# Kernel optimization log

Measured on AMD Instinct MI355X. Metric: run time of the kernel, lower is better.

## Reference

```python
import jax, jax.numpy as jnp
import numpy as np

J = 24          # SMPL_NR_JOINTS
H = 24          # hidden_dim
D_IN = 3        # input_dim (xyz)
SMPL_PARENTS = [-1, 0, 0, 0, 1, 2, 3, 4, 5, 6, 7, 8, 9, 9, 9, 12, 13, 14, 16, 17, 18, 19, 20, 21]

def _build_A():
    # undirected kinematic tree + self loops, row-normalized (mean aggregation)
    M = np.zeros((J, J), np.float32)
    for child, parent in enumerate(SMPL_PARENTS):
        if parent >= 0:
            M[child, parent] = 1.0
            M[parent, child] = 1.0
    M += np.eye(J, dtype=np.float32)
    M /= M.sum(axis=1, keepdims=True)
    return jnp.asarray(M)

A_NORM = _build_A()  # [J, J]

def setup_inputs() -> dict:
    key = jax.random.key(0)
    ks = jax.random.split(key, 12)
    B, S, T = 2048, 24, 24
    g = lambda k, shape, s=0.1: jax.random.normal(k, shape, dtype=jnp.float32) * s
    return {
        "src": g(ks[0], (B, S, J, D_IN), 1.0),
        "tgt": g(ks[1], (B, T, J, D_IN), 1.0),
        "We": g(ks[2], (H, D_IN)), "be": jnp.zeros((H,), jnp.float32),
        # gate order: 0=i, 1=f, 2=c, 3=o
        "Wxl": g(ks[3], (4, H, H)), "bxl": jnp.zeros((4, H), jnp.float32),
        "Wxr": g(ks[4], (4, H, H)),
        "Whl": g(ks[5], (4, H, H)), "bhl": jnp.zeros((4, H), jnp.float32),
        "Whr": g(ks[6], (4, H, H)),
        "wg": g(ks[7], (3, H)),   # peephole weights for i, f, o
        "bg": jnp.zeros((4, H), jnp.float32),
        "Wd": g(ks[8], (D_IN * J, H * J)), "bd": jnp.zeros((D_IN * J,), jnp.float32),
    }

def _gconv(x, Wl, bl, Wr):
    # x: [B, J, D]; mean-aggregate over fixed 24-node graph, then l(agg) + r(x)
    agg = jnp.einsum('ij,bjd->bid', A_NORM, x)
    return agg @ Wl.T + bl + x @ Wr.T

def _cell(X, h, c, Wxl, bxl, Wxr, Whl, bhl, Whr, wg, bg):
    gx = lambda g: _gconv(X, Wxl[g], bxl[g], Wxr[g])
    gh = lambda g: _gconv(h, Whl[g], bhl[g], Whr[g])
    i = jax.nn.sigmoid(gx(0) + gh(0) + wg[0] * c + bg[0])
    f = jax.nn.sigmoid(gx(1) + gh(1) + wg[1] * c + bg[1])
    c_new = f * c + i * jnp.tanh(gx(2) + gh(2) + bg[2])
    o = jax.nn.sigmoid(gx(3) + gh(3) + wg[2] * c_new + bg[3])
    h_new = o * jnp.tanh(c_new)
    return o, h_new, c_new

def reference(src, tgt, We, be, Wxl, bxl, Wxr, Whl, bhl, Whr, wg, bg, Wd, bd):
    B, S = src.shape[0], src.shape[1]
    T = tgt.shape[1]
    params = (Wxl, bxl, Wxr, Whl, bhl, Whr, wg, bg)
    enc = lambda x: jax.nn.relu(x @ We.T + be)  # [B, J, H]

    # --- warm-up over last 24 src frames (deterministic: encode only first step) ---
    X0 = enc(src[:, S - 24])
    h = jnp.zeros((B, J, H), src.dtype)
    c = jnp.zeros((B, J, H), src.dtype)
    out, h, c = _cell(X0, h, c, *params)

    def warm_step(carry, _):
        o_, h_, c_ = carry
        o_, h_, c_ = _cell(o_, h_, c_, *params)
        return (o_, h_, c_), None
    (out, h, c), _ = jax.lax.scan(warm_step, (out, h, c), None, length=23)

    # --- decode T steps: first input is enc(tgt[:,0]), then feed previous out ---
    out0, h, c = _cell(enc(tgt[:, 0]), h, c, *params)

    def dec_step(carry, _):
        o_, h_, c_ = carry
        o2, h2, c2 = _cell(o_, h_, c_, *params)
        return (o2, h2, c2), o2
    _, rest = jax.lax.scan(dec_step, (out0, h, c), None, length=T - 1)  # [T-1, B, J, H]

    seq = jnp.concatenate([out0[None], rest], axis=0)            # [T, B, J, H]
    outs = seq.transpose(1, 0, 2, 3).reshape(B, T, J * H)        # [B, T, 576]
    return outs @ Wd.T + bd                                      # [B, T, 72]
```

## Files before the change

kernel.cpp:

```cpp
#include <hip/hip_runtime.h>


typedef short  s16x8 __attribute__((ext_vector_type(8)));
typedef float  f32x4 __attribute__((ext_vector_type(4)));
typedef _Float16 f16x8 __attribute__((ext_vector_type(8)));

#define TPB 192
#define NB 2
#define PQ_OFF 0
#define UO_OFF 19968
#define SMEM_SZ 26880

#define BAR() do { asm volatile("s_waitcnt lgkmcnt(0)" ::: "memory"); \
                   __builtin_amdgcn_s_barrier(); } while (0)

__device__ __forceinline__ unsigned short f2h(float f) {
    _Float16 h = (_Float16)f;
    return *(unsigned short*)&h;
}
__device__ __forceinline__ unsigned int pkrtz(float a, float b) {
    auto h = __builtin_amdgcn_cvt_pkrtz(a, b);
    return *(unsigned int*)&h;
}
__device__ __forceinline__ float frcp(float x) { return __builtin_amdgcn_rcpf(x); }
__device__ __forceinline__ float sigm(float x) {
    float t = __expf(-x);
    return frcp(1.0f + t);
}
__device__ __forceinline__ float tanh_(float x) {
    float xc = fmaxf(x, -30.f);
    float t = __expf(-2.f * xc);
    return (1.f - t) * frcp(1.f + t);
}

extern "C" __global__ void __launch_bounds__(TPB, 3)
gclstm_main(const float* __restrict__ src,
            const float* __restrict__ tgt,
            const float* __restrict__ We,
            const float* __restrict__ be,
            const float* __restrict__ Wxl,
            const float* __restrict__ bxl,
            const float* __restrict__ Wxr,
            const float* __restrict__ Whl,
            const float* __restrict__ bhl,
            const float* __restrict__ Whr,
            const float* __restrict__ wg,
            const float* __restrict__ bg,
            unsigned short* __restrict__ seqh)
{
    __shared__ __align__(16) char smem[SMEM_SZ];
    unsigned short* PQt  = (unsigned short*)(smem + PQ_OFF);
    unsigned short* UO   = (unsigned short*)(smem + UO_OFF);
    unsigned int*   UO32 = (unsigned int*)(smem + UO_OFF);

    const int tid = threadIdx.x;
    const int b0 = blockIdx.x * NB;
    const int lane = tid & 63, wid = tid >> 6;
    const int l15 = lane & 15, quad = lane >> 4;

    const int par[24] = {-1,0,0,0,1,2,3,4,5,6,7,8,9,9,9,12,13,14,16,17,18,19,20,21};

    f16x8 w1f[4][2];
#pragma unroll
    for (int cj = 0; cj < 4; ++cj) {
        int np = (wid * 4 + cj) * 16 + l15;
        int path = np >= 96 ? 1 : 0;
        int nn = np - path * 96;
        int g = nn / 24, d = nn - g * 24;
        const float* Wx = path ? Wxr : Wxl;
        const float* Wh = path ? Whr : Whl;
#pragma unroll
        for (int kt = 0; kt < 2; ++kt) {
            f16x8 f;
#pragma unroll
            for (int kk = 0; kk < 8; ++kk) {
                int k = kt * 32 + quad * 8 + kk;
                float v = 0.f;
                if (k < 48) {
                    int df = k >> 1;
                    v = (k & 1) ? Wh[g * 576 + d * 24 + df] : Wx[g * 576 + d * 24 + df];
                }
                f[kk] = (_Float16)v;
            }
            w1f[cj][kt] = f;
        }
    }

    f16x8 mf[3];
    {
        int i = wid * 16 + l15;
        int si = i / 24, ji = i - si * 24;
        int cnt = 1 + (par[ji] >= 0 ? 1 : 0);
#pragma unroll
        for (int ch = 0; ch < 24; ++ch) cnt += (par[ch] == ji) ? 1 : 0;
        float cntf = (float)cnt;
#pragma unroll
        for (int kt = 0; kt < 3; ++kt) {
            f16x8 f;
#pragma unroll
            for (int kk = 0; kk < 8; ++kk) {
                int jp = kt * 32 + quad * 8 + kk;
                int sj = jp / 48;
                int rem = jp - sj * 48;
                int pz = rem / 24;
                int j = rem - pz * 24;
                float v = 0.f;
                if (sj == si) {
                    if (pz == 0) v = (j == ji || par[j] == ji || par[ji] == j) ? 1.f : 0.f;
                    else         v = (j == ji) ? cntf : 0.f;
                }
                f[kk] = (_Float16)v;
            }
            mf[kt] = f;
        }
    }

    const int d1 = l15;
    const int d2 = 16 + (l15 & 7);
    const bool lo = l15 < 8;
    float bC1[4], bC2[4], wv1[3], wv2[3];
#pragma unroll
    for (int g = 0; g < 4; ++g) {
        bC1[g] = bxl[g * 24 + d1] + bhl[g * 24 + d1] + bg[g * 24 + d1];
        bC2[g] = bxl[g * 24 + d2] + bhl[g * 24 + d2] + bg[g * 24 + d2];
    }
#pragma unroll
    for (int p = 0; p < 3; ++p) { wv1[p] = wg[p * 24 + d1]; wv2[p] = wg[p * 24 + d2]; }

    int rowR[4];
    float iwR[4];
    unsigned int sb[4];
#pragma unroll
    for (int rr = 0; rr < 4; ++rr) {
        int row = wid * 16 + quad * 4 + rr;
        rowR[rr] = row;
        int j = row % 24;
        int cnt = 1 + (par[j] >= 0 ? 1 : 0);
#pragma unroll
        for (int ch = 0; ch < 24; ++ch) cnt += (par[ch] == j) ? 1 : 0;
        iwR[rr] = cnt == 2 ? 0.5f : cnt == 3 ? (1.f / 3.f) : cnt == 4 ? 0.25f : 0.2f;
        sb[rr] = (unsigned int)((b0 + row / 24) * 13824 + j * 24);
    }
    int row2v[2]; float iw2v[2]; unsigned int sb2v[2];
#pragma unroll
    for (int e = 0; e < 2; ++e) {
        int rsel = lo ? e : e + 2;
        row2v[e] = rowR[rsel]; iw2v[e] = iwR[rsel]; sb2v[e] = sb[rsel];
    }

    float c1[4] = {0.f, 0.f, 0.f, 0.f};
    float c2[2] = {0.f, 0.f};

#pragma unroll
    for (int t = 0; t < 3; ++t) {
        int task = tid + t * TPB;
        int row = task / 12, dp = task - row * 12;
        int b = b0 + row / 24, j = row % 24;
        const float* sp = src + (size_t)b * 1728 + j * 3;
        float s0 = sp[0], s1 = sp[1], s2 = sp[2];
        int d = 2 * dp;
        float x0 = be[d] + s0 * We[d * 3] + s1 * We[d * 3 + 1] + s2 * We[d * 3 + 2];
        float x1 = be[d + 1] + s0 * We[d * 3 + 3] + s1 * We[d * 3 + 4] + s2 * We[d * 3 + 5];
        x0 = fmaxf(x0, 0.f); x1 = fmaxf(x1, 0.f);
        uint2 wv; wv.x = pkrtz(x0, 0.f); wv.y = pkrtz(x1, 0.f);
        *(uint2*)(UO32 + row * 36 + 2 * dp) = wv;
    }
    {
        int row = tid >> 2, c = tid & 3;
        uint2 z; z.x = 0u; z.y = 0u;
        *(uint2*)(UO32 + row * 36 + 24 + 2 * c) = z;
    }
    __syncthreads();

    for (int s = 0; s < 48; ++s) {
        if (s == 24) {
#pragma unroll
            for (int t = 0; t < 3; ++t) {
                int task = tid + t * TPB;
                int row = task / 12, dp = task - row * 12;
                int b = b0 + row / 24, j = row % 24;
                const float* tp = tgt + (size_t)b * 1728 + j * 3;
                float s0 = tp[0], s1 = tp[1], s2 = tp[2];
                int d = 2 * dp;
                float x0 = be[d] + s0 * We[d * 3] + s1 * We[d * 3 + 1] + s2 * We[d * 3 + 2];
                float x1 = be[d + 1] + s0 * We[d * 3 + 3] + s1 * We[d * 3 + 4]
                         + s2 * We[d * 3 + 5];
                x0 = fmaxf(x0, 0.f); x1 = fmaxf(x1, 0.f);
                UO[row * 72 + 4 * dp] = f2h(x0);
                UO[row * 72 + 4 * dp + 2] = f2h(x1);
            }
            BAR();
        }

        f32x4 acc1[3][4];
#pragma unroll
        for (int rt = 0; rt < 3; ++rt)
#pragma unroll
            for (int cj = 0; cj < 4; ++cj) acc1[rt][cj] = (f32x4)0.f;
#pragma unroll
        for (int kt = 0; kt < 2; ++kt) {
            f16x8 a[3];
#pragma unroll
            for (int rt = 0; rt < 3; ++rt)
                a[rt] = *(const f16x8*)(UO + (rt * 16 + l15) * 72 + kt * 32 + quad * 8);
#pragma unroll
            for (int rt = 0; rt < 3; ++rt)
#pragma unroll
                for (int cj = 0; cj < 4; ++cj)
                    acc1[rt][cj] = __builtin_amdgcn_mfma_f32_16x16x32_f16(a[rt], w1f[cj][kt], acc1[rt][cj], 0, 0, 0);
        }
#pragma unroll
        for (int rt = 0; rt < 3; ++rt)
#pragma unroll
            for (int cj = 0; cj < 4; ++cj) {
                int np = (wid * 4 + cj) * 16 + l15;
                int path = np >= 96;
                int nn = np - (path ? 96 : 0);
                int jg = rt * 16 + quad * 4;
                int col = (path ? 24 : 0) + jg + (jg >= 24 ? 24 : 0);
                uint2 wv;
                wv.x = pkrtz(acc1[rt][cj][0], acc1[rt][cj][1]);
                wv.y = pkrtz(acc1[rt][cj][2], acc1[rt][cj][3]);
                *(uint2*)(PQt + nn * 104 + col) = wv;
            }
        BAR();

        f32x4 acc2[6];
#pragma unroll
        for (int nt = 0; nt < 6; ++nt) acc2[nt] = (f32x4)0.f;
#pragma unroll
        for (int kt = 0; kt < 3; ++kt) {
            if (kt == 2 && wid == 0) continue;
            if (kt == 0 && wid == 2) continue;
            f16x8 bf[6];
#pragma unroll
            for (int nt = 0; nt < 6; ++nt)
                bf[nt] = *(const f16x8*)(PQt + (nt * 16 + l15) * 104 + kt * 32 + quad * 8);
#pragma unroll
            for (int nt = 0; nt < 6; ++nt)
                acc2[nt] = __builtin_amdgcn_mfma_f32_16x16x32_f16(mf[kt], bf[nt], acc2[nt], 0, 0, 0);
        }

        const int so = (s - 24) * 576;

#pragma unroll
        for (int rr = 0; rr < 4; ++rr) {
            float pf_s = __shfl_xor(lo ? acc2[2][rr] : acc2[1][rr], 8);
            float po_s = __shfl_xor(lo ? acc2[5][rr] : acc2[4][rr], 8);
            float iw = iwR[rr];
            int row = rowR[rr];
            float c = c1[rr];
            float pi = fmaf(iw, acc2[0][rr], bC1[0]);
            float pf = fmaf(iw, pf_s, bC1[1]);
            float pc = fmaf(iw, acc2[3][rr], bC1[2]);
            float po = fmaf(iw, po_s, bC1[3]);
            float iv = sigm(fmaf(wv1[0], c, pi));
            float fv = sigm(fmaf(wv1[1], c, pf));
            float cn = fmaf(fv, c, iv * tanh_(pc));
            float ov = sigm(fmaf(wv1[2], cn, po));
            c1[rr] = cn;
            float hv = ov * tanh_(cn);
            unsigned int pk = pkrtz(ov, hv);
            UO32[row * 36 + d1] = pk;
            if (s >= 24) seqh[sb[rr] + (unsigned int)(so + d1)] = (unsigned short)pk;
        }
#pragma unroll
        for (int e = 0; e < 2; ++e) {
            float sA = __shfl_xor(lo ? acc2[1][e + 2] : acc2[2][e], 8);
            float sB = __shfl_xor(lo ? acc2[4][e + 2] : acc2[5][e], 8);
            float g0 = lo ? acc2[1][e] : sA;
            float g1 = lo ? sA : acc2[2][e + 2];
            float g2 = lo ? acc2[4][e] : sB;
            float g3 = lo ? sB : acc2[5][e + 2];
            float iw = iw2v[e];
            int row = row2v[e];
            float c = c2[e];
            float pi = fmaf(iw, g0, bC2[0]);
            float pf = fmaf(iw, g1, bC2[1]);
            float pc = fmaf(iw, g2, bC2[2]);
            float po = fmaf(iw, g3, bC2[3]);
            float iv = sigm(fmaf(wv2[0], c, pi));
            float fv = sigm(fmaf(wv2[1], c, pf));
            float cn = fmaf(fv, c, iv * tanh_(pc));
            float ov = sigm(fmaf(wv2[2], cn, po));
            c2[e] = cn;
            float hv = ov * tanh_(cn);
            unsigned int pk = pkrtz(ov, hv);
            UO32[row * 36 + d2] = pk;
            if (s >= 24) seqh[sb2v[e] + (unsigned int)(so + d2)] = (unsigned short)pk;
        }
        BAR();
    }
}

extern "C" __global__ void __launch_bounds__(256)
wd_conv(const float* __restrict__ Wd, unsigned short* __restrict__ WdH)
{
    int i = blockIdx.x * 256 + threadIdx.x;
    if (i < 46080) {
        int n = i / 576, k = i - n * 576;
        WdH[i] = (n < 72) ? f2h(Wd[n * 576 + k]) : (unsigned short)0;
    }
}

__global__ void __launch_bounds__(256, 4)
gclstm_proj_reg(const unsigned short* __restrict__ seqh,
                const unsigned short* __restrict__ WdH,
                const float* __restrict__ bd,
                float* __restrict__ out)
{
    const int tid = threadIdx.x;
    const int R0 = blockIdx.x * 64;
    const int lane = tid & 63, wid = tid >> 6;
    const int l15 = lane & 15, quad = lane >> 4;

    const unsigned short* arow = seqh + (size_t)(R0 + wid * 16 + l15) * 576;
    f32x4 acc[5];
#pragma unroll
    for (int j = 0; j < 5; ++j) acc[j] = (f32x4)0.f;

#pragma unroll
    for (int kc = 0; kc < 576; kc += 96) {
        f16x8 a[3], b[5][3];
#pragma unroll
        for (int kt = 0; kt < 3; ++kt) {
            int koff = kc + kt * 32 + quad * 8;
            a[kt] = *(const f16x8*)(arow + koff);
#pragma unroll
            for (int j = 0; j < 5; ++j)
                b[j][kt] = *(const f16x8*)(WdH + (size_t)(j * 16 + l15) * 576 + koff);
        }
#pragma unroll
        for (int kt = 0; kt < 3; ++kt)
#pragma unroll
            for (int j = 0; j < 5; ++j)
                acc[j] = __builtin_amdgcn_mfma_f32_16x16x32_f16(a[kt], b[j][kt], acc[j], 0, 0, 0);
    }

#pragma unroll
    for (int j = 0; j < 5; ++j) {
        int n = j * 16 + l15;
        if (n < 72) {
            float bv = bd[n];
            int rbase = R0 + wid * 16 + quad * 4;
#pragma unroll
            for (int r = 0; r < 4; ++r)
                out[(size_t)(rbase + r) * 72 + (size_t)n] = acc[j][r] + bv;
        }
    }
}

__global__ void __launch_bounds__(256, 6)
gclstm_proj_lds(const unsigned short* __restrict__ seqh,
                const float* __restrict__ Wd,
                const float* __restrict__ bd,
                float* __restrict__ out)
{
    __shared__ unsigned short SQ[32 * 104];
    __shared__ unsigned short WH[80 * 104];

    const int tid = threadIdx.x;
    const int R0 = blockIdx.x * 32;
    const int lane = tid & 63, wid = tid >> 6;
    const int l15 = lane & 15, quad = lane >> 4;
    const int rt = wid & 1;
    const int c0 = (wid < 2) ? 0 : 3;
    const int nct = (wid < 2) ? 3 : 2;

    f32x4 acc[3];
#pragma unroll
    for (int j = 0; j < 3; ++j) acc[j] = (f32x4)0.f;

    for (int kc = 0; kc < 576; kc += 96) {
        __syncthreads();
        for (int i = tid; i < 384; i += 256) {
            int r = i / 12, c8 = i - r * 12;
            *(s16x8*)(&SQ[r * 104 + c8 * 8]) =
                *(const s16x8*)(seqh + (size_t)(R0 + r) * 576 + (size_t)(kc + c8 * 8));
        }
        for (int i = tid; i < 7680; i += 256) {
            int n = i / 96, kk = i - n * 96;
            float v = (n < 72) ? Wd[(size_t)n * 576 + (size_t)(kc + kk)] : 0.f;
            WH[n * 104 + kk] = f2h(v);
        }
        __syncthreads();
#pragma unroll
        for (int kt = 0; kt < 3; ++kt) {
            int koff = kt * 32 + quad * 8;
            f16x8 a = *(const f16x8*)(&SQ[(rt * 16 + l15) * 104 + koff]);
#pragma unroll
            for (int j = 0; j < 3; ++j) {
                if (j < nct) {
                    f16x8 b = *(const f16x8*)(&WH[((c0 + j) * 16 + l15) * 104 + koff]);
                    acc[j] = __builtin_amdgcn_mfma_f32_16x16x32_f16(a, b, acc[j], 0, 0, 0);
                }
            }
        }
    }

#pragma unroll
    for (int j = 0; j < 3; ++j) {
        if (j < nct) {
            int n = (c0 + j) * 16 + l15;
            if (n < 72) {
                float bv = bd[n];
                int rbase = R0 + rt * 16 + quad * 4;
#pragma unroll
                for (int r = 0; r < 4; ++r)
                    out[(size_t)(rbase + r) * 72 + (size_t)n] = acc[j][r] + bv;
            }
        }
    }
}

extern "C" void kernel_launch(void* const* d_in, const int* in_sizes, int n_in,
                              void* d_out, int out_size, void* d_ws, size_t ws_size,
                              hipStream_t stream)
{
    const float* src = (const float*)d_in[0];
    const float* tgt = (const float*)d_in[1];
    const float* We  = (const float*)d_in[2];
    const float* be  = (const float*)d_in[3];
    const float* Wxl = (const float*)d_in[4];
    const float* bxl = (const float*)d_in[5];
    const float* Wxr = (const float*)d_in[6];
    const float* Whl = (const float*)d_in[7];
    const float* bhl = (const float*)d_in[8];
    const float* Whr = (const float*)d_in[9];
    const float* wg  = (const float*)d_in[10];
    const float* bg  = (const float*)d_in[11];
    const float* Wd  = (const float*)d_in[12];
    const float* bd  = (const float*)d_in[13];
    float* out = (float*)d_out;
    unsigned short* seqh = (unsigned short*)d_ws;

    const size_t seq_bytes = (size_t)2048 * 24 * 576 * 2;
    unsigned short* WdH = (unsigned short*)((char*)d_ws + seq_bytes);
    const bool preconv = ws_size >= seq_bytes + (size_t)80 * 576 * 2;

    if (preconv)
        wd_conv<<<dim3(180), dim3(256), 0, stream>>>(Wd, WdH);
    gclstm_main<<<dim3(1024), dim3(TPB), 0, stream>>>(
        src, tgt, We, be, Wxl, bxl, Wxr, Whl, bhl, Whr, wg, bg, seqh);
    if (preconv)
        gclstm_proj_reg<<<dim3(768), dim3(256), 0, stream>>>(seqh, WdH, bd, out);
    else
        gclstm_proj_lds<<<dim3(1536), dim3(256), 0, stream>>>(seqh, Wd, bd, out);
}
```

Baseline: 352.2 us.

## Fuse output projection into recurrent kernel every eight decode steps

Removes the separate projection kernel and computes the Wd projection inside the main LSTM kernel. Every 8 decode steps the block waits for its global seqh writes, issues a barrier, and runs MFMA over the last 8 timesteps of its 2 samples, reading them back from global memory. This saves a kernel launch and a pass over seqh, but it adds a vmcnt(0) drain plus extra work to the recurrent critical path. It also relies on the block's own global writes being visible to its other waves after a barrier.

```diff
diff --git a/kernel.cpp b/kernel.cpp
--- a/kernel.cpp
+++ b/kernel.cpp
@@ -33,7 +33,8 @@
     return (1.f - t) * frcp(1.f + t);
 }
 
-extern "C" __global__ void __launch_bounds__(TPB, 3)
+template <int FUSE>
+__global__ void __launch_bounds__(TPB, 3)
 gclstm_main(const float* __restrict__ src,
             const float* __restrict__ tgt,
             const float* __restrict__ We,
@@ -46,7 +47,10 @@
             const float* __restrict__ Whr,
             const float* __restrict__ wg,
             const float* __restrict__ bg,
-            unsigned short* __restrict__ seqh)
+            unsigned short* __restrict__ seqh,
+            const unsigned short* __restrict__ WdH,
+            const float* __restrict__ bd,
+            float* __restrict__ out)
 {
     __shared__ __align__(16) char smem[SMEM_SZ];
     unsigned short* PQt  = (unsigned short*)(smem + PQ_OFF);
@@ -147,6 +151,20 @@
         int rsel = lo ? e : e + 2;
         row2v[e] = rowR[rsel]; iw2v[e] = iwR[rsel]; sb2v[e] = sb[rsel];
     }
+
+    const int fnt = (wid < 2) ? 2 : 1;
+    const int fnb = wid * 2;
+    float bdv[2] = {0.f, 0.f};
+    if (FUSE) {
+#pragma unroll
+        for (int jt = 0; jt < 2; ++jt) {
+            int n = (fnb + jt) * 16 + l15;
+            if (jt < fnt && n < 72) bdv[jt] = bd[n];
+        }
+    }
+    const int sampleA = l15 >> 3, tqA = l15 & 7;
+    const unsigned int aoffF =
+        (unsigned int)((b0 + sampleA) * 13824 + tqA * 576);
 
     float c1[4] = {0.f, 0.f, 0.f, 0.f};
     float c2[2] = {0.f, 0.f};
@@ -289,7 +307,50 @@
             UO32[row * 36 + d2] = pk;
             if (s >= 24) seqh[sb2v[e] + (unsigned int)(so + d2)] = (unsigned short)pk;
         }
-        BAR();
+
+        if (FUSE && s >= 31 && (s & 7) == 7) {
+            asm volatile("s_waitcnt vmcnt(0) lgkmcnt(0)" ::: "memory");
+            __builtin_amdgcn_s_barrier();
+            const int tb = s - 31;
+            const unsigned int abase = aoffF + (unsigned int)(tb * 576);
+            f32x4 facc[2];
+            facc[0] = (f32x4)0.f; facc[1] = (f32x4)0.f;
+#pragma unroll
+            for (int kg = 0; kg < 6; ++kg) {
+                f16x8 av[3], bv0[3], bv1[3];
+#pragma unroll
+                for (int ki = 0; ki < 3; ++ki) {
+                    int k = (kg * 3 + ki) * 32 + quad * 8;
+                    av[ki] = *(const f16x8*)(seqh + abase + (unsigned int)k);
+                    bv0[ki] = *(const f16x8*)(WdH + (size_t)(fnb * 16 + l15) * 576 + k);
+                    if (fnt == 2)
+                        bv1[ki] = *(const f16x8*)(WdH + (size_t)((fnb + 1) * 16 + l15) * 576 + k);
+                }
+#pragma unroll
+                for (int ki = 0; ki < 3; ++ki) {
+                    facc[0] = __builtin_amdgcn_mfma_f32_16x16x32_f16(av[ki], bv0[ki], facc[0], 0, 0, 0);
+                    if (fnt == 2)
+                        facc[1] = __builtin_amdgcn_mfma_f32_16x16x32_f16(av[ki], bv1[ki], facc[1], 0, 0, 0);
+                }
+            }
+#pragma unroll
+            for (int jt = 0; jt < 2; ++jt) {
+                if (jt < fnt) {
+                    int n = (fnb + jt) * 16 + l15;
+                    if (n < 72) {
+#pragma unroll
+                        for (int r = 0; r < 4; ++r) {
+                            int ar = quad * 4 + r;
+                            int smp = ar >> 3, tq = ar & 7;
+                            out[(size_t)(b0 + smp) * 1728 + (size_t)((tb + tq) * 72 + n)]
+                                = facc[jt][r] + bdv[jt];
+                        }
+                    }
+                }
+            }
+        } else {
+            BAR();
+        }
     }
 }
 
@@ -300,53 +361,6 @@
     if (i < 46080) {
         int n = i / 576, k = i - n * 576;
         WdH[i] = (n < 72) ? f2h(Wd[n * 576 + k]) : (unsigned short)0;
-    }
-}
-
-__global__ void __launch_bounds__(256, 4)
-gclstm_proj_reg(const unsigned short* __restrict__ seqh,
-                const unsigned short* __restrict__ WdH,
-                const float* __restrict__ bd,
-                float* __restrict__ out)
-{
-    const int tid = threadIdx.x;
-    const int R0 = blockIdx.x * 64;
-    const int lane = tid & 63, wid = tid >> 6;
-    const int l15 = lane & 15, quad = lane >> 4;
-
-    const unsigned short* arow = seqh + (size_t)(R0 + wid * 16 + l15) * 576;
-    f32x4 acc[5];
-#pragma unroll
-    for (int j = 0; j < 5; ++j) acc[j] = (f32x4)0.f;
-
-#pragma unroll
-    for (int kc = 0; kc < 576; kc += 96) {
-        f16x8 a[3], b[5][3];
-#pragma unroll
-        for (int kt = 0; kt < 3; ++kt) {
-            int koff = kc + kt * 32 + quad * 8;
-            a[kt] = *(const f16x8*)(arow + koff);
-#pragma unroll
-            for (int j = 0; j < 5; ++j)
-                b[j][kt] = *(const f16x8*)(WdH + (size_t)(j * 16 + l15) * 576 + koff);
-        }
-#pragma unroll
-        for (int kt = 0; kt < 3; ++kt)
-#pragma unroll
-            for (int j = 0; j < 5; ++j)
-                acc[j] = __builtin_amdgcn_mfma_f32_16x16x32_f16(a[kt], b[j][kt], acc[j], 0, 0, 0);
-    }
-
-#pragma unroll
-    for (int j = 0; j < 5; ++j) {
-        int n = j * 16 + l15;
-        if (n < 72) {
-            float bv = bd[n];
-            int rbase = R0 + wid * 16 + quad * 4;
-#pragma unroll
-            for (int r = 0; r < 4; ++r)
-                out[(size_t)(rbase + r) * 72 + (size_t)n] = acc[j][r] + bv;
-        }
     }
 }
 
@@ -438,12 +452,15 @@
     unsigned short* WdH = (unsigned short*)((char*)d_ws + seq_bytes);
     const bool preconv = ws_size >= seq_bytes + (size_t)80 * 576 * 2;
 
-    if (preconv)
+    if (preconv) {
         wd_conv<<<dim3(180), dim3(256), 0, stream>>>(Wd, WdH);
-    gclstm_main<<<dim3(1024), dim3(TPB), 0, stream>>>(
-        src, tgt, We, be, Wxl, bxl, Wxr, Whl, bhl, Whr, wg, bg, seqh);
-    if (preconv)
-        gclstm_proj_reg<<<dim3(768), dim3(256), 0, stream>>>(seqh, WdH, bd, out);
-    else
+        gclstm_main<1><<<dim3(1024), dim3(TPB), 0, stream>>>(
+            src, tgt, We, be, Wxl, bxl, Wxr, Whl, bhl, Whr, wg, bg,
+            seqh, WdH, bd, out);
+    } else {
+        gclstm_main<0><<<dim3(1024), dim3(TPB), 0, stream>>>(
+            src, tgt, We, be, Wxl, bxl, Wxr, Whl, bhl, Whr, wg, bg,
+            seqh, nullptr, bd, out);
         gclstm_proj_lds<<<dim3(1536), dim3(256), 0, stream>>>(seqh, Wd, bd, out);
-}
+    }
+}
```

New measurement: 414.8 us. +17.8%, slower.
